# Kernel optimization log

Measured on AMD Instinct MI355X. Metric: run time of the kernel, lower is better.

The kernel has to match this reference:

```python
import jax, jax.numpy as jnp
import numpy as np

NEG_SLOPE = 0.2  # PyG GATConv leaky_relu negative_slope


def gat_conv(x, src, dst, W, att_src, att_dst, bias, heads, out_c, concat):
    """PyG-style GATConv (eval mode, dropout off). src/dst include self-loops.
    x: [N, F_in]; W: [F_in, heads*out_c]; att_*: [heads, out_c]; bias: [heads*out_c] or [out_c].
    """
    N = x.shape[0]
    h = (x @ W).reshape(N, heads, out_c)                       # [N, H, C]
    a_src = jnp.einsum('nhc,hc->nh', h, att_src)               # [N, H]
    a_dst = jnp.einsum('nhc,hc->nh', h, att_dst)               # [N, H]
    e = jax.nn.leaky_relu(a_src[src] + a_dst[dst], NEG_SLOPE)  # [E, H]
    # softmax over incoming edges per destination node
    m = jax.ops.segment_max(e, dst, num_segments=N)            # [N, H]
    ex = jnp.exp(e - m[dst])                                   # [E, H]
    s = jax.ops.segment_sum(ex, dst, num_segments=N)           # [N, H]
    alpha = ex / (s[dst] + 1e-16)                              # [E, H]
    msg = alpha[:, :, None] * h[src]                           # [E, H, C]
    out = jax.ops.segment_sum(msg, dst, num_segments=N)        # [N, H, C]
    if concat:
        out = out.reshape(N, heads * out_c)
    else:
        out = out.mean(axis=1)
    return out + bias


def setup_inputs() -> dict:
    key = jax.random.key(0)
    ks = jax.random.split(key, 10)
    N, E, F_in, H, C, OUT = 100000, 800000, 128, 8, 16, 2
    sc1 = 1.0 / np.sqrt(F_in)
    sc2 = 1.0 / np.sqrt(H * C)
    return {
        'x': jax.random.normal(ks[0], (N, F_in), dtype=jnp.float32),
        'edge_index': jax.random.randint(ks[1], (2, E), 0, N, dtype=jnp.int64),
        'W1': jax.random.normal(ks[2], (F_in, H * C), dtype=jnp.float32) * sc1,
        'att_src1': jax.random.normal(ks[3], (H, C), dtype=jnp.float32) * sc1,
        'att_dst1': jax.random.normal(ks[4], (H, C), dtype=jnp.float32) * sc1,
        'b1': jnp.zeros((H * C,), dtype=jnp.float32),
        'W2': jax.random.normal(ks[5], (H * C, OUT), dtype=jnp.float32) * sc2,
        'att_src2': jax.random.normal(ks[6], (1, OUT), dtype=jnp.float32) * sc2,
        'att_dst2': jax.random.normal(ks[7], (1, OUT), dtype=jnp.float32) * sc2,
        'b2': jnp.zeros((OUT,), dtype=jnp.float32),
    }


def reference(x, edge_index, W1, att_src1, att_dst1, b1, W2, att_src2, att_dst2, b2):
    N = x.shape[0]
    loops = jnp.arange(N, dtype=edge_index.dtype)
    src = jnp.concatenate([edge_index[0], loops])  # PyG add_self_loops=True
    dst = jnp.concatenate([edge_index[1], loops])
    h = gat_conv(x, src, dst, W1, att_src1, att_dst1, b1, heads=8, out_c=16, concat=True)
    h = jax.nn.elu(h)
    # F.dropout in eval mode is identity
    out = gat_conv(h, src, dst, W2, att_src2, att_dst2, b2, heads=1, out_c=2, concat=False)
    return out
```

## Files before the change

### kernel.cpp

```cpp
#include <hip/hip_runtime.h>
#include <hip/hip_bf16.h>
#include <math.h>

#define NEG_SLOPE 0.2f

typedef short bf16x8 __attribute__((ext_vector_type(8)));
typedef float f32x4 __attribute__((ext_vector_type(4)));
typedef float f32x2 __attribute__((ext_vector_type(2)));
typedef _Float16 f16x2 __attribute__((ext_vector_type(2)));

__device__ __forceinline__ float lrelu(float x) { return fmaxf(x, NEG_SLOPE * x); }

__device__ __forceinline__ ushort f2bf(float f) {
  __hip_bfloat16 b = __float2bfloat16(f);
  return *reinterpret_cast<ushort*>(&b);
}

__device__ __forceinline__ unsigned char f2fp8(float f) {
  return (unsigned char)(__builtin_amdgcn_cvt_pk_fp8_f32(f, f, 0, false) & 0xFF);
}

__device__ __forceinline__ f16x2 fp8x2_f16x2(unsigned w) {
#if defined(__has_builtin) && __has_builtin(__builtin_amdgcn_cvt_pk_f16_fp8)
  return __builtin_amdgcn_cvt_pk_f16_fp8((short)w);
#else
  f32x2 p = __builtin_amdgcn_cvt_pk_f32_fp8(w, 0);
  return (f16x2){(_Float16)p[0], (_Float16)p[1]};
#endif
}

__global__ __launch_bounds__(256) void k_prep(
    const float* __restrict__ W1, const float* __restrict__ ats1, const float* __restrict__ atd1,
    ushort* __restrict__ Wg, int* __restrict__ deg, int N)
{
  int t = blockIdx.x * 256 + threadIdx.x;
  if (t < N) deg[t] = 0;
  if (t < 128 * 128) {
    int k = t >> 7, n = t & 127;
    Wg[(size_t)n * 128 + (k ^ ((n & 7) << 3))] = f2bf(W1[t]);
  } else if (t < 128 * 128 + 128 * 16) {
    int tt = t - 128 * 128;
    int k = tt >> 4;
    int c = tt & 15;
    int head = c & 7;
    const float* av = (c < 8) ? ats1 : atd1;
    float s = 0.f;
#pragma unroll
    for (int ch = 0; ch < 16; ++ch)
      s += W1[k * 128 + head * 16 + ch] * av[head * 16 + ch];
    int n = 128 + c;
    Wg[(size_t)n * 128 + (k ^ ((n & 7) << 3))] = f2bf(s);
  }
}

__global__ __launch_bounds__(256) void k_gemm1m(
    const float* __restrict__ x, const ushort* __restrict__ Wg,
    unsigned char* __restrict__ h1f, float* __restrict__ as1, float* __restrict__ ad1, int N)
{
  __shared__ ushort Wls[144 * 128];
  const int tid = threadIdx.x;
  const float4* Wg4 = (const float4*)Wg;
  float4* Wl4 = (float4*)Wls;
#pragma unroll
  for (int i = 0; i < 9; ++i) Wl4[tid + i * 256] = Wg4[tid + i * 256];
  __syncthreads();

  const int lane = tid & 63, wid = tid >> 6;
  const int r0 = blockIdx.x * 64 + wid * 16;
  const int lr = lane & 15, kg = lane >> 4;
  int row = r0 + lr; if (row >= N) row = N - 1;
  const float* xr = x + (size_t)row * 128;

  f32x4 acc[9];
#pragma unroll
  for (int i = 0; i < 9; ++i) acc[i] = (f32x4){0.f, 0.f, 0.f, 0.f};

#pragma unroll
  for (int ks = 0; ks < 4; ++ks) {
    int k0 = ks * 32 + kg * 8;
    float4 xa = *(const float4*)(xr + k0);
    float4 xb = *(const float4*)(xr + k0 + 4);
    bf16x8 af;
    af[0] = f2bf(xa.x); af[1] = f2bf(xa.y); af[2] = f2bf(xa.z); af[3] = f2bf(xa.w);
    af[4] = f2bf(xb.x); af[5] = f2bf(xb.y); af[6] = f2bf(xb.z); af[7] = f2bf(xb.w);
#pragma unroll
    for (int nt = 0; nt < 9; ++nt) {
      int n = nt * 16 + lr;
      bf16x8 bfr = *(const bf16x8*)(Wls + n * 128 + (k0 ^ ((n & 7) << 3)));
      acc[nt] = __builtin_amdgcn_mfma_f32_16x16x32_bf16(af, bfr, acc[nt], 0, 0, 0);
    }
  }
#pragma unroll
  for (int nt = 0; nt < 8; ++nt) {
#pragma unroll
    for (int i = 0; i < 4; ++i) {
      int r = r0 + kg * 4 + i;
      if (r < N) h1f[(size_t)r * 128 + nt * 16 + lr] = f2fp8(acc[nt][i]);
    }
  }
#pragma unroll
  for (int i = 0; i < 4; ++i) {
    int r = r0 + kg * 4 + i;
    if (r < N) {
      if (lr < 8) as1[(size_t)r * 8 + lr]     = acc[8][i];
      else        ad1[(size_t)r * 8 + lr - 8] = acc[8][i];
    }
  }
}

__global__ __launch_bounds__(256) void k_hist(const int* __restrict__ ei, int E, int N,
                                              int* __restrict__ deg, int* __restrict__ lrank) {
  int e = blockIdx.x * 256 + threadIdx.x;
  if (e >= E + N) return;
  int d = (e < E) ? ei[E + e] : e - E;
  lrank[e] = atomicAdd(&deg[d], 1);
}

__global__ __launch_bounds__(256) void k_scan1(const int* __restrict__ deg,
                                               int* __restrict__ rowptr,
                                               int* __restrict__ bsum, int N) {
  __shared__ int sc[256];
  int b = blockIdx.x, t = threadIdx.x;
  int i0 = b * 512 + 2 * t, i1 = i0 + 1;
  int a = (i0 < N) ? deg[i0] : 0;
  int bb = (i1 < N) ? deg[i1] : 0;
  int s = a + bb;
  sc[t] = s; __syncthreads();
  int run = s;
  for (int dd = 1; dd < 256; dd <<= 1) {
    int v = (t >= dd) ? sc[t - dd] : 0; __syncthreads();
    run += v; sc[t] = run; __syncthreads();
  }
  int excl = run - s;
  if (i0 < N) rowptr[i0] = excl;
  if (i1 < N) rowptr[i1] = excl + a;
  if (t == 255) bsum[b] = run;
}

__global__ __launch_bounds__(256) void k_scan2(int* __restrict__ bsum, int nb) {
  __shared__ int sc[256];
  int t = threadIdx.x;
  int s = (t < nb) ? bsum[t] : 0;
  sc[t] = s; __syncthreads();
  int run = s;
  for (int dd = 1; dd < 256; dd <<= 1) {
    int v = (t >= dd) ? sc[t - dd] : 0; __syncthreads();
    run += v; sc[t] = run; __syncthreads();
  }
  if (t < nb) bsum[t] = run - s;
}

__global__ __launch_bounds__(256) void k_scan3(int* __restrict__ rowptr,
                                               const int* __restrict__ bsum, int N) {
  int i = blockIdx.x * 256 + threadIdx.x;
  if (i >= N) return;
  rowptr[i] += bsum[i >> 9];
}

__global__ __launch_bounds__(256) void k_place(const int* __restrict__ ei, int E, int N,
                                               const int* __restrict__ rowptr,
                                               const int* __restrict__ lrank,
                                               int* __restrict__ srt) {
  int e = blockIdx.x * 256 + threadIdx.x;
  if (e >= E + N) return;
  int s, d;
  if (e < E) { s = ei[e]; d = ei[E + e]; } else { s = d = e - E; }
  srt[rowptr[d] + lrank[e]] = s;
}

__global__ __launch_bounds__(256) void k_agg1f(
    const int* __restrict__ rowptr, const int* __restrict__ deg, const int* __restrict__ srt,
    const float* __restrict__ as1, const float* __restrict__ ad1,
    const unsigned char* __restrict__ h1f,
    const float* __restrict__ b1, const float* __restrict__ W2,
    const float* __restrict__ ats2, const float* __restrict__ atd2,
    float4* __restrict__ nd2, int N)
{
  const int lane = threadIdx.x & 63;
  const int wid = threadIdx.x >> 6;
  const int grp = lane >> 4, l16 = lane & 15;
  const int d0 = blockIdx.x * 16 + wid * 4 + grp;
  const int d = min(d0, N - 1);
  const int hh = l16 >> 1;
  const int hoff = 8 * l16;

  const int start = rowptr[d];
  const int dg = deg[d];
  const int dgm1 = dg - 1;
  const int* sp = srt + start;
  const float adh = ad1[d * 8 + hh];

  f16x2 ac0 = {0, 0}, ac1 = {0, 0}, ac2 = {0, 0}, ac3 = {0, 0};
  float sum = 0.f;

#define EDGEACC(hv, ah) { \
    f16x2 av2 = {(ah), (ah)}; \
    ac0 += fp8x2_f16x2((hv).x & 0xffffu) * av2; \
    ac1 += fp8x2_f16x2((hv).x >> 16)     * av2; \
    ac2 += fp8x2_f16x2((hv).y & 0xffffu) * av2; \
    ac3 += fp8x2_f16x2((hv).y >> 16)     * av2; \
  }

  int c = 0;
  int s0 = sp[0];
  int s1 = sp[min(1, dgm1)];
  int s2 = sp[min(2, dgm1)];
  int s3 = sp[min(3, dgm1)];
  while (c < dg) {
    int cn = c + 4;
    int t0 = sp[min(cn,     dgm1)];
    int t1 = sp[min(cn + 1, dgm1)];
    int t2 = sp[min(cn + 2, dgm1)];
    int t3 = sp[min(cn + 3, dgm1)];
    float a0v = as1[s0 * 8 + hh];
    uint2 hv0 = *(const uint2*)(h1f + s0 * 128 + hoff);
    float a1v = as1[s1 * 8 + hh];
    uint2 hv1 = *(const uint2*)(h1f + s1 * 128 + hoff);
    float a2v = as1[s2 * 8 + hh];
    uint2 hv2 = *(const uint2*)(h1f + s2 * 128 + hoff);
    float a3v = as1[s3 * 8 + hh];
    uint2 hv3 = *(const uint2*)(h1f + s3 * 128 + hoff);

    float u0f = __expf(lrelu(a0v + adh));
    float u1f = (c + 1 < dg) ? __expf(lrelu(a1v + adh)) : 0.f;
    float u2f = (c + 2 < dg) ? __expf(lrelu(a2v + adh)) : 0.f;
    float u3f = (c + 3 < dg) ? __expf(lrelu(a3v + adh)) : 0.f;
    sum += (u0f + u1f) + (u2f + u3f);
    _Float16 u0 = (_Float16)u0f, u1 = (_Float16)u1f;
    _Float16 u2 = (_Float16)u2f, u3 = (_Float16)u3f;
    EDGEACC(hv0, u0);
    EDGEACC(hv1, u1);
    EDGEACC(hv2, u2);
    EDGEACC(hv3, u3);

    c = cn; s0 = t0; s1 = t1; s2 = t2; s3 = t3;
  }
#undef EDGEACC

  float v[8] = {(float)ac0[0], (float)ac0[1], (float)ac1[0], (float)ac1[1],
                (float)ac2[0], (float)ac2[1], (float)ac3[0], (float)ac3[1]};
  const float inv = 1.f / (sum + 1e-16f);

  float4 b0 = *(const float4*)(b1 + hoff);
  float4 b4 = *(const float4*)(b1 + hoff + 4);
  v[0] = fmaf(v[0], inv, b0.x); v[1] = fmaf(v[1], inv, b0.y);
  v[2] = fmaf(v[2], inv, b0.z); v[3] = fmaf(v[3], inv, b0.w);
  v[4] = fmaf(v[4], inv, b4.x); v[5] = fmaf(v[5], inv, b4.y);
  v[6] = fmaf(v[6], inv, b4.z); v[7] = fmaf(v[7], inv, b4.w);
#pragma unroll
  for (int j = 0; j < 8; ++j) v[j] = v[j] > 0.f ? v[j] : (__expf(v[j]) - 1.f);

  const float4* W24 = (const float4*)(W2 + 16 * l16);
  float4 w0 = W24[0], w1 = W24[1], w2 = W24[2], w3 = W24[3];
  float p0 = v[0]*w0.x + v[1]*w0.z + v[2]*w1.x + v[3]*w1.z
           + v[4]*w2.x + v[5]*w2.z + v[6]*w3.x + v[7]*w3.z;
  float p1 = v[0]*w0.y + v[1]*w0.w + v[2]*w1.y + v[3]*w1.w
           + v[4]*w2.y + v[5]*w2.w + v[6]*w3.y + v[7]*w3.w;
#pragma unroll
  for (int m = 1; m < 16; m <<= 1) { p0 += __shfl_xor(p0, m); p1 += __shfl_xor(p1, m); }
  if (l16 == 0 && d0 < N) {
    float a2 = p0 * ats2[0] + p1 * ats2[1];
    float dd2 = p0 * atd2[0] + p1 * atd2[1];
    nd2[d0] = make_float4(p0, p1, a2, dd2);
  }
}

__global__ __launch_bounds__(256) void k_agg2f(
    const int* __restrict__ rowptr, const int* __restrict__ deg, const int* __restrict__ srt,
    const float4* __restrict__ nd2, const float* __restrict__ b2,
    float* __restrict__ out, int N)
{
  const int l16 = threadIdx.x & 15;
  const int d = blockIdx.x * 16 + (threadIdx.x >> 4);
  if (d >= N) return;
  const int start = rowptr[d];
  const int dg = deg[d];
  const float adv = nd2[d].w;

  float se = 0.f, a0 = 0.f, a1 = 0.f;
  for (int c = l16; c < dg; c += 16) {
    int s = srt[start + c];
    float4 r = nd2[s];
    float ex = __expf(lrelu(r.z + adv));
    se += ex;
    a0 = fmaf(ex, r.x, a0);
    a1 = fmaf(ex, r.y, a1);
  }
#pragma unroll
  for (int m = 1; m < 16; m <<= 1) {
    se += __shfl_xor(se, m, 16);
    a0 += __shfl_xor(a0, m, 16);
    a1 += __shfl_xor(a1, m, 16);
  }
  if (l16 == 0) {
    float invs = 1.f / (se + 1e-16f);
    out[(size_t)d * 2]     = a0 * invs + b2[0];
    out[(size_t)d * 2 + 1] = a1 * invs + b2[1];
  }
}

extern "C" void kernel_launch(void* const* d_in, const int* in_sizes, int n_in,
                              void* d_out, int out_size, void* d_ws, size_t ws_size,
                              hipStream_t stream) {
  const float* x    = (const float*)d_in[0];
  const int*   ei   = (const int*)d_in[1];
  const float* W1   = (const float*)d_in[2];
  const float* ats1 = (const float*)d_in[3];
  const float* atd1 = (const float*)d_in[4];
  const float* b1   = (const float*)d_in[5];
  const float* W2   = (const float*)d_in[6];
  const float* ats2 = (const float*)d_in[7];
  const float* atd2 = (const float*)d_in[8];
  const float* b2   = (const float*)d_in[9];
  float* out = (float*)d_out;

  const int N  = in_sizes[0] / 128;
  const int E  = in_sizes[1] / 2;
  const int E2 = E + N;
  const int nb = (N + 511) / 512;

  float* ws = (float*)d_ws;
  size_t off = 0;
  unsigned char* h1f = (unsigned char*)(ws + off); off += (size_t)N * 32;
  float* as1 = ws + off; off += (size_t)N * 8;
  float* ad1 = ws + off; off += (size_t)N * 8;
  float4* nd2 = (float4*)(ws + off); off += (size_t)N * 4;
  int* deg    = (int*)(ws + off); off += (size_t)N;
  int* rowptr = (int*)(ws + off); off += (size_t)N;
  int* bsum   = (int*)(ws + off); off += 256;
  int* srt    = (int*)(ws + off); off += (size_t)E2;
  int* lrank  = (int*)(ws + off); off += (size_t)E2;
  ushort* Wg  = (ushort*)(ws + off); off += 144 * 64;

  const int prep_blocks = max((128 * 128 + 128 * 16 + 255) / 256, (N + 255) / 256);
  k_prep<<<prep_blocks, 256, 0, stream>>>(W1, ats1, atd1, Wg, deg, N);

  k_gemm1m<<<(N + 63) / 64, 256, 0, stream>>>(x, Wg, h1f, as1, ad1, N);

  k_hist<<<(E2 + 255) / 256, 256, 0, stream>>>(ei, E, N, deg, lrank);
  k_scan1<<<nb, 256, 0, stream>>>(deg, rowptr, bsum, N);
  k_scan2<<<1, 256, 0, stream>>>(bsum, nb);
  k_scan3<<<(N + 255) / 256, 256, 0, stream>>>(rowptr, bsum, N);
  k_place<<<(E2 + 255) / 256, 256, 0, stream>>>(ei, E, N, rowptr, lrank, srt);

  k_agg1f<<<(N + 15) / 16, 256, 0, stream>>>(rowptr, deg, srt, as1, ad1, h1f,
                                             b1, W2, ats2, atd2, nd2, N);

  k_agg2f<<<(N + 15) / 16, 256, 0, stream>>>(rowptr, deg, srt, nd2, b2, out, N);
}
```

Baseline: 121.7 us.

## Replace three-kernel scan with single-pass decoupled lookback and store as1 in fp16

Merges the three scan kernels (block scan, block-sum scan, add-back) into one decoupled-lookback kernel. Each block publishes its aggregate or inclusive prefix to a status array that k_prep clears, and removes two launches plus a pass over rowptr. Separately, the per-node source attention logits are stored as fp16 instead of fp32, which halves the gather traffic for as1 in the aggregation loop. The cost is a serial spin on block predecessors, which assumes forward progress of earlier blocks, and reduced precision in the attention logits.

```diff
diff --git a/kernel.cpp b/kernel.cpp
--- a/kernel.cpp
+++ b/kernel.cpp
@@ -31,10 +31,11 @@
 
 __global__ __launch_bounds__(256) void k_prep(
     const float* __restrict__ W1, const float* __restrict__ ats1, const float* __restrict__ atd1,
-    ushort* __restrict__ Wg, int* __restrict__ deg, int N)
+    ushort* __restrict__ Wg, int* __restrict__ deg, int* __restrict__ status, int N)
 {
   int t = blockIdx.x * 256 + threadIdx.x;
   if (t < N) deg[t] = 0;
+  if (t < 256) status[t] = 0;
   if (t < 128 * 128) {
     int k = t >> 7, n = t & 127;
     Wg[(size_t)n * 128 + (k ^ ((n & 7) << 3))] = f2bf(W1[t]);
@@ -55,7 +56,8 @@
 
 __global__ __launch_bounds__(256) void k_gemm1m(
     const float* __restrict__ x, const ushort* __restrict__ Wg,
-    unsigned char* __restrict__ h1f, float* __restrict__ as1, float* __restrict__ ad1, int N)
+    unsigned char* __restrict__ h1f, _Float16* __restrict__ as1h,
+    float* __restrict__ ad1, int N)
 {
   __shared__ ushort Wls[144 * 128];
   const int tid = threadIdx.x;
@@ -102,7 +104,7 @@
   for (int i = 0; i < 4; ++i) {
     int r = r0 + kg * 4 + i;
     if (r < N) {
-      if (lr < 8) as1[(size_t)r * 8 + lr]     = acc[8][i];
+      if (lr < 8) as1h[(size_t)r * 8 + lr]    = (_Float16)acc[8][i];
       else        ad1[(size_t)r * 8 + lr - 8] = acc[8][i];
     }
   }
@@ -116,13 +118,15 @@
   lrank[e] = atomicAdd(&deg[d], 1);
 }
 
-__global__ __launch_bounds__(256) void k_scan1(const int* __restrict__ deg,
-                                               int* __restrict__ rowptr,
-                                               int* __restrict__ bsum, int N) {
+__global__ __launch_bounds__(256) void k_scan_lb(
+    const int* __restrict__ deg, int* __restrict__ rowptr,
+    int* __restrict__ status, int N)
+{
   __shared__ int sc[256];
-  int b = blockIdx.x, t = threadIdx.x;
-  int i0 = b * 512 + 2 * t, i1 = i0 + 1;
-  int a = (i0 < N) ? deg[i0] : 0;
+  __shared__ int sbase;
+  const int b = blockIdx.x, t = threadIdx.x;
+  const int i0 = b * 512 + 2 * t, i1 = i0 + 1;
+  int a  = (i0 < N) ? deg[i0] : 0;
   int bb = (i1 < N) ? deg[i1] : 0;
   int s = a + bb;
   sc[t] = s; __syncthreads();
@@ -131,30 +135,31 @@
     int v = (t >= dd) ? sc[t - dd] : 0; __syncthreads();
     run += v; sc[t] = run; __syncthreads();
   }
-  int excl = run - s;
-  if (i0 < N) rowptr[i0] = excl;
-  if (i1 < N) rowptr[i1] = excl + a;
-  if (t == 255) bsum[b] = run;
-}
-
-__global__ __launch_bounds__(256) void k_scan2(int* __restrict__ bsum, int nb) {
-  __shared__ int sc[256];
-  int t = threadIdx.x;
-  int s = (t < nb) ? bsum[t] : 0;
-  sc[t] = s; __syncthreads();
-  int run = s;
-  for (int dd = 1; dd < 256; dd <<= 1) {
-    int v = (t >= dd) ? sc[t - dd] : 0; __syncthreads();
-    run += v; sc[t] = run; __syncthreads();
-  }
-  if (t < nb) bsum[t] = run - s;
-}
-
-__global__ __launch_bounds__(256) void k_scan3(int* __restrict__ rowptr,
-                                               const int* __restrict__ bsum, int N) {
-  int i = blockIdx.x * 256 + threadIdx.x;
-  if (i >= N) return;
-  rowptr[i] += bsum[i >> 9];
+  const int excl = run - s;
+  const int total = sc[255];
+
+  if (t == 0) {
+    if (b > 0)
+      __hip_atomic_store(&status[b], (total << 2) | 1, __ATOMIC_RELEASE, __HIP_MEMORY_SCOPE_AGENT);
+    int base = 0;
+    if (b > 0) {
+      int j = b - 1;
+      while (true) {
+        int st = __hip_atomic_load(&status[j], __ATOMIC_ACQUIRE, __HIP_MEMORY_SCOPE_AGENT);
+        int fl = st & 3;
+        if (fl == 0) continue;
+        base += (st >> 2);
+        if (fl == 2) break;
+        --j;
+      }
+    }
+    __hip_atomic_store(&status[b], ((base + total) << 2) | 2, __ATOMIC_RELEASE, __HIP_MEMORY_SCOPE_AGENT);
+    sbase = base;
+  }
+  __syncthreads();
+  const int gb = sbase;
+  if (i0 < N) rowptr[i0] = gb + excl;
+  if (i1 < N) rowptr[i1] = gb + excl + a;
 }
 
 __global__ __launch_bounds__(256) void k_place(const int* __restrict__ ei, int E, int N,
@@ -170,7 +175,7 @@
 
 __global__ __launch_bounds__(256) void k_agg1f(
     const int* __restrict__ rowptr, const int* __restrict__ deg, const int* __restrict__ srt,
-    const float* __restrict__ as1, const float* __restrict__ ad1,
+    const _Float16* __restrict__ as1h, const float* __restrict__ ad1,
     const unsigned char* __restrict__ h1f,
     const float* __restrict__ b1, const float* __restrict__ W2,
     const float* __restrict__ ats2, const float* __restrict__ atd2,
@@ -212,26 +217,24 @@
     int t1 = sp[min(cn + 1, dgm1)];
     int t2 = sp[min(cn + 2, dgm1)];
     int t3 = sp[min(cn + 3, dgm1)];
-    float a0v = as1[s0 * 8 + hh];
+    _Float16 a0h = as1h[s0 * 8 + hh];
     uint2 hv0 = *(const uint2*)(h1f + s0 * 128 + hoff);
-    float a1v = as1[s1 * 8 + hh];
+    _Float16 a1h = as1h[s1 * 8 + hh];
     uint2 hv1 = *(const uint2*)(h1f + s1 * 128 + hoff);
-    float a2v = as1[s2 * 8 + hh];
+    _Float16 a2h = as1h[s2 * 8 + hh];
     uint2 hv2 = *(const uint2*)(h1f + s2 * 128 + hoff);
-    float a3v = as1[s3 * 8 + hh];
+    _Float16 a3h = as1h[s3 * 8 + hh];
     uint2 hv3 = *(const uint2*)(h1f + s3 * 128 + hoff);
 
-    float u0f = __expf(lrelu(a0v + adh));
-    float u1f = (c + 1 < dg) ? __expf(lrelu(a1v + adh)) : 0.f;
-    float u2f = (c + 2 < dg) ? __expf(lrelu(a2v + adh)) : 0.f;
-    float u3f = (c + 3 < dg) ? __expf(lrelu(a3v + adh)) : 0.f;
+    float u0f = __expf(lrelu((float)a0h + adh));
+    float u1f = (c + 1 < dg) ? __expf(lrelu((float)a1h + adh)) : 0.f;
+    float u2f = (c + 2 < dg) ? __expf(lrelu((float)a2h + adh)) : 0.f;
+    float u3f = (c + 3 < dg) ? __expf(lrelu((float)a3h + adh)) : 0.f;
     sum += (u0f + u1f) + (u2f + u3f);
-    _Float16 u0 = (_Float16)u0f, u1 = (_Float16)u1f;
-    _Float16 u2 = (_Float16)u2f, u3 = (_Float16)u3f;
-    EDGEACC(hv0, u0);
-    EDGEACC(hv1, u1);
-    EDGEACC(hv2, u2);
-    EDGEACC(hv3, u3);
+    EDGEACC(hv0, (_Float16)u0f);
+    EDGEACC(hv1, (_Float16)u1f);
+    EDGEACC(hv2, (_Float16)u2f);
+    EDGEACC(hv3, (_Float16)u3f);
 
     c = cn; s0 = t0; s1 = t1; s2 = t2; s3 = t3;
   }
@@ -322,28 +325,26 @@
   float* ws = (float*)d_ws;
   size_t off = 0;
   unsigned char* h1f = (unsigned char*)(ws + off); off += (size_t)N * 32;
-  float* as1 = ws + off; off += (size_t)N * 8;
+  _Float16* as1h = (_Float16*)(ws + off); off += (size_t)N * 4;
   float* ad1 = ws + off; off += (size_t)N * 8;
   float4* nd2 = (float4*)(ws + off); off += (size_t)N * 4;
   int* deg    = (int*)(ws + off); off += (size_t)N;
   int* rowptr = (int*)(ws + off); off += (size_t)N;
-  int* bsum   = (int*)(ws + off); off += 256;
+  int* status = (int*)(ws + off); off += 256;
   int* srt    = (int*)(ws + off); off += (size_t)E2;
   int* lrank  = (int*)(ws + off); off += (size_t)E2;
   ushort* Wg  = (ushort*)(ws + off); off += 144 * 64;
 
   const int prep_blocks = max((128 * 128 + 128 * 16 + 255) / 256, (N + 255) / 256);
-  k_prep<<<prep_blocks, 256, 0, stream>>>(W1, ats1, atd1, Wg, deg, N);
-
-  k_gemm1m<<<(N + 63) / 64, 256, 0, stream>>>(x, Wg, h1f, as1, ad1, N);
+  k_prep<<<prep_blocks, 256, 0, stream>>>(W1, ats1, atd1, Wg, deg, status, N);
+
+  k_gemm1m<<<(N + 63) / 64, 256, 0, stream>>>(x, Wg, h1f, as1h, ad1, N);
 
   k_hist<<<(E2 + 255) / 256, 256, 0, stream>>>(ei, E, N, deg, lrank);
-  k_scan1<<<nb, 256, 0, stream>>>(deg, rowptr, bsum, N);
-  k_scan2<<<1, 256, 0, stream>>>(bsum, nb);
-  k_scan3<<<(N + 255) / 256, 256, 0, stream>>>(rowptr, bsum, N);
+  k_scan_lb<<<nb, 256, 0, stream>>>(deg, rowptr, status, N);
   k_place<<<(E2 + 255) / 256, 256, 0, stream>>>(ei, E, N, rowptr, lrank, srt);
 
-  k_agg1f<<<(N + 15) / 16, 256, 0, stream>>>(rowptr, deg, srt, as1, ad1, h1f,
+  k_agg1f<<<(N + 15) / 16, 256, 0, stream>>>(rowptr, deg, srt, as1h, ad1, h1f,
                                              b1, W2, ats2, atd2, nd2, N);
 
   k_agg2f<<<(N + 15) / 16, 256, 0, stream>>>(rowptr, deg, srt, nd2, b2, out, N);
```

After: 153.6 us. +26.2%, slower.
